# Performance work log

Measured on AMD Instinct MI355X. Metric: run time of the kernel, lower is better.

## Reference

```python
import jax, jax.numpy as jnp
import numpy as np

# Dia-style ANE decoder dims
B, D, S = 2, 2048, 128          # batch, n_embd, query seqlen
A, T = 1536, 512                # audio_length (self KV cache), text_length (cross KV)
HQ, HKV, HD = 16, 4, 128        # gqa query heads, kv heads, gqa head dim
HC, HDC = 16, 128               # cross-attn heads / head dim (encoder n_head/head_dim)
FF, L = 8192, 2                 # mlp hidden, n_layers
NEG = -3e4                      # large-negative additive mask (stands in for -inf)
EPS = 1e-5


def _rmsnorm(x, w):
    # x: (B, D, S); ANERMSNorm normalizes over channel dim (dim=1)
    inv = jax.lax.rsqrt(jnp.mean(x * x, axis=1, keepdims=True) + EPS)
    return x * inv * w[None, :, None]


def _rope(x, sin, cos):
    # x: (B, H, hd, S); sin/cos: (B, 1, hd//2, S) -- split-half rotary
    h = x.shape[2] // 2
    x1, x2 = x[:, :, :h], x[:, :, h:]
    return jnp.concatenate([x1 * cos - x2 * sin, x2 * cos + x1 * sin], axis=2)


def setup_inputs() -> dict:
    key = jax.random.key(0)
    ks = jax.random.split(key, 16)
    w0 = 256  # KV cache write position
    x = jax.random.normal(ks[0], (B, D, 1, S), jnp.float32)
    positions = (w0 + jnp.arange(S, dtype=jnp.int32))[None, :].repeat(B, axis=0)
    kv_write_index = jnp.array([w0], dtype=jnp.int32)
    # additive causal mask over cache positions: allow cache_pos <= w0 + q_pos
    allowed = jnp.arange(A)[None, :] <= (w0 + jnp.arange(S))[:, None]  # (S, A)
    self_attn_mask = jnp.where(allowed, 0.0, NEG).astype(jnp.float32)[None, None].repeat(B, axis=0)
    encoder_lengths = jnp.full((B, 1), 384, dtype=jnp.int32)
    sc = 0.02
    return {
        'x': x, 'positions': positions, 'kv_write_index': kv_write_index,
        'self_attn_mask': self_attn_mask, 'encoder_lengths': encoder_lengths,
        'q_w': jax.random.normal(ks[1], (L, D, HQ * HD)) * sc,
        'k_w': jax.random.normal(ks[2], (L, D, HKV * HD)) * sc,
        'v_w': jax.random.normal(ks[3], (L, D, HKV * HD)) * sc,
        'o_w': jax.random.normal(ks[4], (L, HQ * HD, D)) * sc,
        'cq_w': jax.random.normal(ks[5], (L, D, HC * HDC)) * sc,
        'co_w': jax.random.normal(ks[6], (L, HC * HDC, D)) * sc,
        'sa_norm_w': jnp.ones((L, D)), 'ca_norm_w': jnp.ones((L, D)),
        'mlp_norm_w': jnp.ones((L, D)), 'final_norm_w': jnp.ones((D,)),
        'wg_w': jax.random.normal(ks[7], (L, D, FF)) * sc,
        'wu_w': jax.random.normal(ks[8], (L, D, FF)) * sc,
        'wd_w': jax.random.normal(ks[9], (L, FF, D)) * sc,
        'k_cache': jax.random.normal(ks[10], (L * B, HKV, A, HD)) * 0.1,
        'v_cache': jax.random.normal(ks[11], (L * B, HKV, HD, A)) * 0.1,
        'ck_cache': jax.random.normal(ks[12], (L * B, HC, T, HDC)) * 0.1,
        'cv_cache': jax.random.normal(ks[13], (L * B, HC, HDC, T)) * 0.1,
    }


def _forward(x4, positions, kv_write_index, self_attn_mask, encoder_lengths,
             q_w, k_w, v_w, o_w, cq_w, co_w, sa_norm_w, ca_norm_w, mlp_norm_w,
             final_norm_w, wg_w, wu_w, wd_w, k_cache, v_cache, ck_cache, cv_cache):
    x = x4[:, :, 0, :]  # (B, D, S) channels-first ANE layout
    w = kv_write_index[0]
    # rotary tables from positions
    inv_freq = 1.0 / (10000.0 ** (jnp.arange(0, HD, 2, dtype=jnp.float32) / HD))
    ang = positions.astype(jnp.float32)[:, None, :] * inv_freq[None, :, None]  # (B, HD/2, S)
    sin, cos = jnp.sin(ang)[:, None], jnp.cos(ang)[:, None]  # (B,1,HD/2,S)
    sa_mask = jnp.swapaxes(self_attn_mask, -1, -2)  # (B,1,A,S), additive
    # cross-attn key padding mask from encoder lengths (non-causal)
    k_valid = jnp.arange(T)[None, :] < encoder_lengths[:, 0:1]  # (B, T)
    ca_mask = jnp.where(k_valid, 0.0, NEG).astype(x.dtype)[:, None, :, None]  # (B,1,T,1)
    scale = 1.0 / np.sqrt(HD).astype(np.float32)
    cscale = 1.0 / np.sqrt(HDC).astype(np.float32)
    G = HQ // HKV
    for l in range(L):
        # ---- self attention with RoPE + KV-cache write ----
        h = _rmsnorm(x, sa_norm_w[l])
        q = jnp.einsum('bds,de->bes', h, q_w[l]).reshape(B, HQ, HD, S)
        k = jnp.einsum('bds,de->bes', h, k_w[l]).reshape(B, HKV, HD, S)
        v = jnp.einsum('bds,de->bes', h, v_w[l]).reshape(B, HKV, HD, S)
        q = _rope(q, sin, cos)
        k = jnp.swapaxes(_rope(k, sin, cos), -1, -2)  # (B,HKV,S,HD)
        k_cache = jax.lax.dynamic_update_slice(k_cache, k, (l * B, 0, w, 0))
        v_cache = jax.lax.dynamic_update_slice(v_cache, v, (l * B, 0, 0, w))
        key = k_cache[l * B:(l + 1) * B]   # (B,HKV,A,HD)
        val = v_cache[l * B:(l + 1) * B]   # (B,HKV,HD,A)
        qg = q.reshape(B, HKV, G, HD, S)
        scores = jnp.einsum('bkad,bkgds->bkgas', key, qg) * scale
        probs = jax.nn.softmax(scores + sa_mask[:, :, None], axis=3)
        attn = jnp.einsum('bkda,bkgas->bkgds', val, probs).reshape(B, HQ * HD, S)
        x = x + jnp.einsum('bes,ed->bds', attn, o_w[l])
        # ---- cross attention (precomputed encoder KV cache, RoPE on q) ----
        h = _rmsnorm(x, ca_norm_w[l])
        q = jnp.einsum('bds,de->bes', h, cq_w[l]).reshape(B, HC, HDC, S)
        q = _rope(q, sin, cos)
        ckey = ck_cache[l * B:(l + 1) * B]  # (B,HC,T,HDC)
        cval = cv_cache[l * B:(l + 1) * B]  # (B,HC,HDC,T)
        cscores = jnp.einsum('bhtd,bhds->bhts', ckey, q) * cscale
        cprobs = jax.nn.softmax(cscores + ca_mask, axis=2)
        cattn = jnp.einsum('bhdt,bhts->bhds', cval, cprobs).reshape(B, HC * HDC, S)
        x = x + jnp.einsum('bes,ed->bds', cattn, co_w[l])
        # ---- SwiGLU MLP ----
        h = _rmsnorm(x, mlp_norm_w[l])
        gate = jnp.einsum('bds,df->bfs', h, wg_w[l])
        up = jnp.einsum('bds,df->bfs', h, wu_w[l])
        x = x + jnp.einsum('bfs,fd->bds', jax.nn.silu(gate) * up, wd_w[l])
    x = _rmsnorm(x, final_norm_w)
    return x[:, :, None, :]


def reference(x, positions, kv_write_index, self_attn_mask, encoder_lengths,
              q_w, k_w, v_w, o_w, cq_w, co_w, sa_norm_w, ca_norm_w, mlp_norm_w,
              final_norm_w, wg_w, wu_w, wd_w, k_cache, v_cache, ck_cache, cv_cache):
    return _forward(x, positions, kv_write_index, self_attn_mask, encoder_lengths,
                    q_w, k_w, v_w, o_w, cq_w, co_w, sa_norm_w, ca_norm_w, mlp_norm_w,
                    final_norm_w, wg_w, wu_w, wd_w, k_cache, v_cache, ck_cache, cv_cache)
```

## Files before the change

kernel.cpp:

```cpp
#include <hip/hip_runtime.h>
#include <math.h>
#include <stdint.h>

namespace {

constexpr int B_ = 2, D_ = 2048, S_ = 128, A_ = 1536, T_ = 512;
constexpr int HQ_ = 16, HKV_ = 4, HD_ = 128, FF_ = 8192, L_ = 2;
constexpr float NEG_ = -30000.0f, EPS_ = 1e-5f;
constexpr int TOK_ = B_ * S_;

typedef __attribute__((ext_vector_type(4))) float f32x4;
typedef __attribute__((ext_vector_type(8))) short s16x8;

__device__ __forceinline__ uint32_t bf16pair(float x) {
  uint32_t xi = __float_as_uint(x);
  uint32_t hi = (xi + 0x7FFFu + ((xi >> 16) & 1u)) >> 16;
  float hf = __uint_as_float(hi << 16);
  float r = x - hf;
  uint32_t ri = __float_as_uint(r);
  uint32_t lo = (ri + 0x7FFFu + ((ri >> 16) & 1u)) >> 16;
  return (hi & 0xFFFFu) | (lo << 16);
}

__device__ __forceinline__ void unpack8(uint4 q0, uint4 q1, s16x8& hi, s16x8& lo) {
  union U { uint32_t w[4]; s16x8 v; };
  U h, l;
  uint32_t u[8] = {q0.x, q0.y, q0.z, q0.w, q1.x, q1.y, q1.z, q1.w};
#pragma unroll
  for (int r = 0; r < 4; r++) {
    h.w[r] = __builtin_amdgcn_perm(u[2 * r + 1], u[2 * r], 0x05040100u);
    l.w[r] = __builtin_amdgcn_perm(u[2 * r + 1], u[2 * r], 0x07060302u);
  }
  hi = h.v;
  lo = l.v;
}

__global__ __launch_bounds__(256) void rms_sumsq(const float* __restrict__ x,
                                                 float* __restrict__ rsum) {
  int b = blockIdx.y, c = blockIdx.x;
  int tid = threadIdx.x;
  int s = tid & 127, dd = tid >> 7;
  const float* xp = x + ((size_t)b * D_ + c * 128) * S_ + s;
  float acc = 0.f;
  for (int d = dd; d < 128; d += 2) {
    float v = xp[(size_t)d * S_];
    acc += v * v;
  }
  __shared__ float lds[256];
  lds[tid] = acc;
  __syncthreads();
  if (dd == 0) atomicAdd(&rsum[b * S_ + s], lds[s] + lds[128 + s]);
}

__global__ __launch_bounds__(256) void rms_apply(const float* __restrict__ x,
                                                 const float* __restrict__ rsum,
                                                 const float* __restrict__ w,
                                                 float* __restrict__ out) {
  int i = blockIdx.x * 256 + threadIdx.x;
  int s = i & (S_ - 1);
  int d = (i / S_) & (D_ - 1);
  int b = i / (D_ * S_);
  float inv = rsqrtf(rsum[b * S_ + s] * (1.0f / D_) + EPS_);
  out[i] = x[i] * inv * w[d];
}

__global__ __launch_bounds__(256) void pack_h(const float* __restrict__ H,
                                              uint32_t* __restrict__ Ht, int K) {
  int b = blockIdx.y;
  int k0 = blockIdx.x * 64;
  __shared__ uint32_t t[128][65];
  int tid = threadIdx.x;
  int s = tid & 127, kk = tid >> 7;
  const float* Hp = H + ((size_t)b * K + k0) * S_ + s;
  for (int k = kk; k < 64; k += 2) t[s][k] = bf16pair(Hp[(size_t)k * S_]);
  __syncthreads();
  int k2 = tid & 63, s2 = tid >> 6;
  uint32_t* Op = Ht + (size_t)(b * S_) * K + k0 + k2;
  for (int ss = s2; ss < 128; ss += 4) Op[(size_t)ss * K] = t[ss][k2];
}

__global__ __launch_bounds__(256, 2) void gemm_mfma(
    const float* __restrict__ W, const uint32_t* __restrict__ Ht,
    float* __restrict__ Out, int M, int K, int KC, int accum) {
  __shared__ uint32_t As[128 * 32];
  __shared__ uint32_t Bs[128 * 32];
  int m0 = blockIdx.x * 128;
  int b = blockIdx.y;
  int k0 = blockIdx.z * KC;
  int tid = threadIdx.x;
  int lane = tid & 63, wave = tid >> 6;
  int wm = (wave >> 1) * 64, wn = (wave & 1) * 64;
  int lr = lane & 15, lg = lane >> 4;
  int a_k4 = (tid >> 5) * 4;
  int a_m4 = (tid & 31) * 4;
  int ag = a_k4 >> 2;
  int b_g = tid & 3;
  int b_s = tid >> 2;
  const uint32_t* HtB = Ht + (size_t)(b * S_) * K;

  f32x4 acc[4][4];
  f32x4 zero = {0.f, 0.f, 0.f, 0.f};
#pragma unroll
  for (int i = 0; i < 4; i++)
#pragma unroll
    for (int j = 0; j < 4; j++) acc[i][j] = zero;

  for (int kk = k0; kk < k0 + KC; kk += 32) {
    const float* Wp = W + (size_t)(kk + a_k4) * M + (m0 + a_m4);
    float4 w0 = *(const float4*)(Wp);
    float4 w1 = *(const float4*)(Wp + (size_t)M);
    float4 w2 = *(const float4*)(Wp + 2 * (size_t)M);
    float4 w3 = *(const float4*)(Wp + 3 * (size_t)M);
    {
      uint4 u;
      int m = a_m4;
      u.x = bf16pair(w0.x); u.y = bf16pair(w1.x); u.z = bf16pair(w2.x); u.w = bf16pair(w3.x);
      *(uint4*)&As[m * 32 + ((ag ^ (m & 7)) << 2)] = u;
      m = a_m4 + 1;
      u.x = bf16pair(w0.y); u.y = bf16pair(w1.y); u.z = bf16pair(w2.y); u.w = bf16pair(w3.y);
      *(uint4*)&As[m * 32 + ((ag ^ (m & 7)) << 2)] = u;
      m = a_m4 + 2;
      u.x = bf16pair(w0.z); u.y = bf16pair(w1.z); u.z = bf16pair(w2.z); u.w = bf16pair(w3.z);
      *(uint4*)&As[m * 32 + ((ag ^ (m & 7)) << 2)] = u;
      m = a_m4 + 3;
      u.x = bf16pair(w0.w); u.y = bf16pair(w1.w); u.z = bf16pair(w2.w); u.w = bf16pair(w3.w);
      *(uint4*)&As[m * 32 + ((ag ^ (m & 7)) << 2)] = u;
    }
#pragma unroll
    for (int c = 0; c < 2; c++)
#pragma unroll
      for (int d = 0; d < 2; d++) {
        int s = b_s + c * 64;
        int g = b_g + d * 4;
        uint4 v = *(const uint4*)&HtB[(size_t)s * K + kk + g * 4];
        *(uint4*)&Bs[s * 32 + ((g ^ (s & 7)) << 2)] = v;
      }
    __syncthreads();
    s16x8 ah[4], al[4], bhf[4], blf[4];
#pragma unroll
    for (int mi = 0; mi < 4; mi++) {
      int row = wm + mi * 16 + lr;
      const uint32_t* p = &As[row * 32];
      uint4 q0 = *(const uint4*)&p[(((lg << 1) ^ (row & 7)) << 2)];
      uint4 q1 = *(const uint4*)&p[((((lg << 1) | 1) ^ (row & 7)) << 2)];
      unpack8(q0, q1, ah[mi], al[mi]);
    }
#pragma unroll
    for (int ni = 0; ni < 4; ni++) {
      int row = wn + ni * 16 + lr;
      const uint32_t* p = &Bs[row * 32];
      uint4 q0 = *(const uint4*)&p[(((lg << 1) ^ (row & 7)) << 2)];
      uint4 q1 = *(const uint4*)&p[((((lg << 1) | 1) ^ (row & 7)) << 2)];
      unpack8(q0, q1, bhf[ni], blf[ni]);
    }
#pragma unroll
    for (int mi = 0; mi < 4; mi++)
#pragma unroll
      for (int ni = 0; ni < 4; ni++)
        acc[mi][ni] = __builtin_amdgcn_mfma_f32_16x16x32_bf16(ah[mi], bhf[ni],
                                                              acc[mi][ni], 0, 0, 0);
#pragma unroll
    for (int mi = 0; mi < 4; mi++)
#pragma unroll
      for (int ni = 0; ni < 4; ni++)
        acc[mi][ni] = __builtin_amdgcn_mfma_f32_16x16x32_bf16(ah[mi], blf[ni],
                                                              acc[mi][ni], 0, 0, 0);
#pragma unroll
    for (int mi = 0; mi < 4; mi++)
#pragma unroll
      for (int ni = 0; ni < 4; ni++)
        acc[mi][ni] = __builtin_amdgcn_mfma_f32_16x16x32_bf16(al[mi], bhf[ni],
                                                              acc[mi][ni], 0, 0, 0);
    __syncthreads();
  }
  if (gridDim.z == 1) {
#pragma unroll
    for (int mi = 0; mi < 4; mi++)
#pragma unroll
      for (int ni = 0; ni < 4; ni++) {
        int m = m0 + wm + mi * 16 + lg * 4;
        int sI = wn + ni * 16 + lr;
        size_t base = ((size_t)b * M + m) * S_ + sI;
#pragma unroll
        for (int r = 0; r < 4; r++) {
          float v = acc[mi][ni][r];
          if (accum) v += Out[base + (size_t)r * S_];
          Out[base + (size_t)r * S_] = v;
        }
      }
  } else {
#pragma unroll
    for (int mi = 0; mi < 4; mi++)
#pragma unroll
      for (int ni = 0; ni < 4; ni++) {
        int m = m0 + wm + mi * 16 + lg * 4;
        int sI = wn + ni * 16 + lr;
        size_t base = ((size_t)b * M + m) * S_ + sI;
#pragma unroll
        for (int r = 0; r < 4; r++)
          atomicAdd(&Out[base + (size_t)r * S_], acc[mi][ni][r]);
      }
  }
}

__global__ __launch_bounds__(256, 2) void attn_scores_mfma(
    const float* __restrict__ key, const uint32_t* __restrict__ Qt,
    float* __restrict__ P, const float* __restrict__ maskArr,
    const int* __restrict__ encLen, const int* __restrict__ wptr, float scale,
    int gshift, int AN, int mode) {
  int bh = blockIdx.y;
  int b = bh >> 4, h = bh & 15;
  int kvh = h >> gshift, nkv = 16 >> gshift;
  int Aeff = (mode == 0) ? (wptr[0] + S_) : T_;
  int a0 = blockIdx.x * 128;
  if (a0 >= Aeff) return;
  __shared__ uint32_t As[128 * 32];
  __shared__ uint32_t Bs[128 * 32];
  const float* kbase =
      key + (size_t)(b * nkv + kvh) * AN * HD_ + (size_t)a0 * HD_;
  const uint32_t* qbase = Qt + (size_t)(b * S_) * D_ + h * HD_;
  int tid = threadIdx.x, lane = tid & 63, wave = tid >> 6;
  int wm = (wave >> 1) * 64, wn = (wave & 1) * 64;
  int lr = lane & 15, lg = lane >> 4;
  int g_ = tid & 3, r_ = tid >> 2;

  f32x4 acc[4][4];
  f32x4 zero = {0.f, 0.f, 0.f, 0.f};
#pragma unroll
  for (int i = 0; i < 4; i++)
#pragma unroll
    for (int j = 0; j < 4; j++) acc[i][j] = zero;

  for (int hc = 0; hc < HD_; hc += 32) {
#pragma unroll
    for (int c = 0; c < 2; c++)
#pragma unroll
      for (int d = 0; d < 2; d++) {
        int row = r_ + c * 64, g = g_ + d * 4;
        float4 v = *(const float4*)&kbase[(size_t)row * HD_ + hc + g * 4];
        uint4 u;
        u.x = bf16pair(v.x); u.y = bf16pair(v.y);
        u.z = bf16pair(v.z); u.w = bf16pair(v.w);
        *(uint4*)&As[row * 32 + ((g ^ (row & 7)) << 2)] = u;
        uint4 q = *(const uint4*)&qbase[(size_t)row * D_ + hc + g * 4];
        *(uint4*)&Bs[row * 32 + ((g ^ (row & 7)) << 2)] = q;
      }
    __syncthreads();
    s16x8 ah[4], al[4], bhf[4], blf[4];
#pragma unroll
    for (int mi = 0; mi < 4; mi++) {
      int row = wm + mi * 16 + lr;
      const uint32_t* p = &As[row * 32];
      uint4 q0 = *(const uint4*)&p[(((lg << 1) ^ (row & 7)) << 2)];
      uint4 q1 = *(const uint4*)&p[((((lg << 1) | 1) ^ (row & 7)) << 2)];
      unpack8(q0, q1, ah[mi], al[mi]);
    }
#pragma unroll
    for (int ni = 0; ni < 4; ni++) {
      int row = wn + ni * 16 + lr;
      const uint32_t* p = &Bs[row * 32];
      uint4 q0 = *(const uint4*)&p[(((lg << 1) ^ (row & 7)) << 2)];
      uint4 q1 = *(const uint4*)&p[((((lg << 1) | 1) ^ (row & 7)) << 2)];
      unpack8(q0, q1, bhf[ni], blf[ni]);
    }
#pragma unroll
    for (int mi = 0; mi < 4; mi++)
#pragma unroll
      for (int ni = 0; ni < 4; ni++)
        acc[mi][ni] = __builtin_amdgcn_mfma_f32_16x16x32_bf16(ah[mi], bhf[ni],
                                                              acc[mi][ni], 0, 0, 0);
#pragma unroll
    for (int mi = 0; mi < 4; mi++)
#pragma unroll
      for (int ni = 0; ni < 4; ni++)
        acc[mi][ni] = __builtin_amdgcn_mfma_f32_16x16x32_bf16(ah[mi], blf[ni],
                                                              acc[mi][ni], 0, 0, 0);
#pragma unroll
    for (int mi = 0; mi < 4; mi++)
#pragma unroll
      for (int ni = 0; ni < 4; ni++)
        acc[mi][ni] = __builtin_amdgcn_mfma_f32_16x16x32_bf16(al[mi], bhf[ni],
                                                              acc[mi][ni], 0, 0, 0);
    __syncthreads();
  }
  int eLen = (mode == 0) ? 0 : encLen[b];
#pragma unroll
  for (int mi = 0; mi < 4; mi++)
#pragma unroll
    for (int ni = 0; ni < 4; ni++) {
      int ab = a0 + wm + mi * 16 + lg * 4;
      int s = wn + ni * 16 + lr;
      float* Pp = P + ((size_t)bh * S_ + s) * T_;
      const float* Mp = maskArr + ((size_t)b * S_ + s) * A_;
#pragma unroll
      for (int r = 0; r < 4; r++) {
        int a = ab + r;
        if (a < Aeff) {
          float mval = (mode == 0) ? Mp[a] : ((a < eLen) ? 0.f : NEG_);
          Pp[a] = acc[mi][ni][r] * scale + mval;
        }
      }
    }
}

__global__ __launch_bounds__(256, 2) void attn_pv_mfma(
    const float* __restrict__ val, const float* __restrict__ P,
    float* __restrict__ out, const int* __restrict__ wptr, int gshift, int AN,
    int mode) {
  int bh = blockIdx.x;
  int b = bh >> 4, h = bh & 15;
  int kvh = h >> gshift, nkv = 16 >> gshift;
  int Aeff = (mode == 0) ? (wptr[0] + S_) : T_;
  int nk = (Aeff + 31) >> 5;
  __shared__ uint32_t As[128 * 32];
  __shared__ uint32_t Bs[128 * 32];
  const float* vbase = val + (size_t)(b * nkv + kvh) * HD_ * AN;
  const float* Pb = P + (size_t)bh * S_ * T_;
  int tid = threadIdx.x, lane = tid & 63, wave = tid >> 6;
  int wm = (wave >> 1) * 64, wn = (wave & 1) * 64;
  int lr = lane & 15, lg = lane >> 4;
  int g_ = tid & 3, r_ = tid >> 2;

  f32x4 acc[4][4];
  f32x4 zero = {0.f, 0.f, 0.f, 0.f};
#pragma unroll
  for (int i = 0; i < 4; i++)
#pragma unroll
    for (int j = 0; j < 4; j++) acc[i][j] = zero;

  for (int kkt = 0; kkt < nk; kkt++) {
    int a0c = kkt * 32;
#pragma unroll
    for (int c = 0; c < 2; c++)
#pragma unroll
      for (int d = 0; d < 2; d++) {
        int row = r_ + c * 64, g = g_ + d * 4;
        int a = a0c + g * 4;
        float4 v = *(const float4*)&vbase[(size_t)row * AN + a];
        uint4 u;
        u.x = bf16pair(v.x); u.y = bf16pair(v.y);
        u.z = bf16pair(v.z); u.w = bf16pair(v.w);
        *(uint4*)&As[row * 32 + ((g ^ (row & 7)) << 2)] = u;
        float4 p4 = *(const float4*)&Pb[(size_t)row * T_ + a];
        uint4 up;
        up.x = (a + 0 < Aeff) ? bf16pair(p4.x) : 0u;
        up.y = (a + 1 < Aeff) ? bf16pair(p4.y) : 0u;
        up.z = (a + 2 < Aeff) ? bf16pair(p4.z) : 0u;
        up.w = (a + 3 < Aeff) ? bf16pair(p4.w) : 0u;
        *(uint4*)&Bs[row * 32 + ((g ^ (row & 7)) << 2)] = up;
      }
    __syncthreads();
    s16x8 ah[4], al[4], bhf[4], blf[4];
#pragma unroll
    for (int mi = 0; mi < 4; mi++) {
      int row = wm + mi * 16 + lr;
      const uint32_t* p = &As[row * 32];
      uint4 q0 = *(const uint4*)&p[(((lg << 1) ^ (row & 7)) << 2)];
      uint4 q1 = *(const uint4*)&p[((((lg << 1) | 1) ^ (row & 7)) << 2)];
      unpack8(q0, q1, ah[mi], al[mi]);
    }
#pragma unroll
    for (int ni = 0; ni < 4; ni++) {
      int row = wn + ni * 16 + lr;
      const uint32_t* p = &Bs[row * 32];
      uint4 q0 = *(const uint4*)&p[(((lg << 1) ^ (row & 7)) << 2)];
      uint4 q1 = *(const uint4*)&p[((((lg << 1) | 1) ^ (row & 7)) << 2)];
      unpack8(q0, q1, bhf[ni], blf[ni]);
    }
#pragma unroll
    for (int mi = 0; mi < 4; mi++)
#pragma unroll
      for (int ni = 0; ni < 4; ni++)
        acc[mi][ni] = __builtin_amdgcn_mfma_f32_16x16x32_bf16(ah[mi], bhf[ni],
                                                              acc[mi][ni], 0, 0, 0);
#pragma unroll
    for (int mi = 0; mi < 4; mi++)
#pragma unroll
      for (int ni = 0; ni < 4; ni++)
        acc[mi][ni] = __builtin_amdgcn_mfma_f32_16x16x32_bf16(ah[mi], blf[ni],
                                                              acc[mi][ni], 0, 0, 0);
#pragma unroll
    for (int mi = 0; mi < 4; mi++)
#pragma unroll
      for (int ni = 0; ni < 4; ni++)
        acc[mi][ni] = __builtin_amdgcn_mfma_f32_16x16x32_bf16(al[mi], bhf[ni],
                                                              acc[mi][ni], 0, 0, 0);
    __syncthreads();
  }
#pragma unroll
  for (int mi = 0; mi < 4; mi++)
#pragma unroll
    for (int ni = 0; ni < 4; ni++) {
      int hd = wm + mi * 16 + lg * 4;
      int s = wn + ni * 16 + lr;
      size_t base = ((size_t)bh * HD_ + hd) * S_ + s;
#pragma unroll
      for (int r = 0; r < 4; r++) out[base + (size_t)r * S_] = acc[mi][ni][r];
    }
}

__device__ __forceinline__ void rope_angles(int pos, int i, float& sn, float& cs) {
  float inv_freq = powf(10000.0f, -(float)i * (1.0f / 64.0f));
  float ang = (float)pos * inv_freq;
  sn = sinf(ang);
  cs = cosf(ang);
}

__global__ __launch_bounds__(256) void rope_q(float* __restrict__ q,
                                              const int* __restrict__ positions) {
  int idx = blockIdx.x * 256 + threadIdx.x;
  int s = idx & 127;
  int i = (idx >> 7) & 63;
  int b = idx >> 17;
  float sn, cs;
  rope_angles(positions[b * S_ + s], i, sn, cs);
  size_t o1 = (size_t)(idx >> 13) * (128 * S_) + (size_t)i * S_ + s;
  float x1 = q[o1], x2 = q[o1 + 64 * S_];
  q[o1] = x1 * cs - x2 * sn;
  q[o1 + 64 * S_] = x2 * cs + x1 * sn;
}

__global__ __launch_bounds__(256) void rope_k_store(const float* __restrict__ kbuf,
                                                    const int* __restrict__ positions,
                                                    const int* __restrict__ wptr,
                                                    float* __restrict__ k_cache, int l) {
  int idx = blockIdx.x * 256 + threadIdx.x;
  int i = idx & 63;
  int s = (idx >> 6) & 127;
  int kv = (idx >> 13) & 3;
  int b = idx >> 15;
  int w = wptr[0];
  float sn, cs;
  rope_angles(positions[b * S_ + s], i, sn, cs);
  size_t i1 = ((size_t)(b * HKV_ + kv) * HD_ + i) * S_ + s;
  float x1 = kbuf[i1], x2 = kbuf[i1 + 64 * S_];
  size_t o = ((size_t)((l * B_ + b) * HKV_ + kv) * A_ + (w + s)) * HD_ + i;
  k_cache[o] = x1 * cs - x2 * sn;
  k_cache[o + 64] = x2 * cs + x1 * sn;
}

__global__ __launch_bounds__(256) void store_v(const float* __restrict__ vbuf,
                                               const int* __restrict__ wptr,
                                               float* __restrict__ v_cache, int l) {
  int idx = blockIdx.x * 256 + threadIdx.x;
  int s = idx & 127;
  int hd = (idx >> 7) & 127;
  int kv = (idx >> 14) & 3;
  int b = idx >> 16;
  int w = wptr[0];
  v_cache[((size_t)((l * B_ + b) * HKV_ + kv) * HD_ + hd) * A_ + w + s] = vbuf[idx];
}

__global__ __launch_bounds__(128) void softmax_rows(float* __restrict__ P,
                                                    const int* __restrict__ wptr,
                                                    int mode) {
  int row = blockIdx.x;
  int Aeff = (mode == 0) ? (wptr[0] + S_) : T_;
  float* p = P + (size_t)row * T_;
  int tid = threadIdx.x;
  float v[4];
  int cnt = 0;
  float m = -1e30f;
  for (int a = tid; a < Aeff; a += 128) {
    float t = p[a];
    v[cnt++] = t;
    m = fmaxf(m, t);
  }
  __shared__ float r0[2], r1[2];
  for (int off = 32; off > 0; off >>= 1) m = fmaxf(m, __shfl_down(m, off));
  if ((tid & 63) == 0) r0[tid >> 6] = m;
  __syncthreads();
  m = fmaxf(r0[0], r0[1]);
  float sum = 0.f;
  for (int i = 0; i < cnt; i++) {
    v[i] = expf(v[i] - m);
    sum += v[i];
  }
  for (int off = 32; off > 0; off >>= 1) sum += __shfl_down(sum, off);
  if ((tid & 63) == 0) r1[tid >> 6] = sum;
  __syncthreads();
  float inv = 1.f / (r1[0] + r1[1]);
  cnt = 0;
  for (int a = tid; a < Aeff; a += 128) p[a] = v[cnt++] * inv;
}

__global__ __launch_bounds__(256) void silu_mul(float* __restrict__ gate,
                                                const float* __restrict__ up) {
  int i = blockIdx.x * 256 + threadIdx.x;
  float g = gate[i];
  gate[i] = g / (1.f + expf(-g)) * up[i];
}

}

extern "C" void kernel_launch(void* const* d_in, const int* in_sizes, int n_in,
                              void* d_out, int out_size, void* d_ws, size_t ws_size,
                              hipStream_t stream) {
  const float* x_in = (const float*)d_in[0];
  const int* positions = (const int*)d_in[1];
  const int* wptr = (const int*)d_in[2];
  const float* maskArr = (const float*)d_in[3];
  const int* encLen = (const int*)d_in[4];
  const float* q_w = (const float*)d_in[5];
  const float* k_w = (const float*)d_in[6];
  const float* v_w = (const float*)d_in[7];
  const float* o_w = (const float*)d_in[8];
  const float* cq_w = (const float*)d_in[9];
  const float* co_w = (const float*)d_in[10];
  const float* sa_norm = (const float*)d_in[11];
  const float* ca_norm = (const float*)d_in[12];
  const float* mlp_norm = (const float*)d_in[13];
  const float* fin_norm = (const float*)d_in[14];
  const float* wg_w = (const float*)d_in[15];
  const float* wu_w = (const float*)d_in[16];
  const float* wd_w = (const float*)d_in[17];
  float* k_cache = (float*)d_in[18];
  float* v_cache = (float*)d_in[19];
  const float* ck_cache = (const float*)d_in[20];
  const float* cv_cache = (const float*)d_in[21];
  float* out = (float*)d_out;

  float* ws = (float*)d_ws;
  const size_t BDS = (size_t)B_ * D_ * S_;
  float* X = ws;
  float* Hb = X + BDS;
  float* Q = Hb + BDS;
  float* Attn = Q + BDS;
  float* Kb = Attn + BDS;
  float* Vb = Kb + (size_t)B_ * 512 * S_;
  float* Pbuf = Vb + (size_t)B_ * 512 * S_;
  float* Up = Pbuf + (size_t)B_ * 16 * S_ * T_;
  float* Rsum = Up + (size_t)B_ * FF_ * S_;
  uint32_t* Ht = (uint32_t*)(Rsum + B_ * S_);

  const float scale = 0.08838834764831845f;

  hipMemcpyAsync(X, x_in, BDS * sizeof(float), hipMemcpyDeviceToDevice, stream);

  auto rms = [&](const float* src, const float* w, float* dst) {
    hipMemsetAsync(Rsum, 0, B_ * S_ * sizeof(float), stream);
    rms_sumsq<<<dim3(16, B_), 256, 0, stream>>>(src, Rsum);
    rms_apply<<<dim3(B_ * D_ * S_ / 256), 256, 0, stream>>>(src, Rsum, w, dst);
  };
  auto pack = [&](const float* src, int K) {
    pack_h<<<dim3(K / 64, B_), 256, 0, stream>>>(src, Ht, K);
  };
  auto mgemm = [&](const float* Wm, float* Outm, int M, int K, int SK, int accum,
                   int zero) {
    if (zero)
      hipMemsetAsync(Outm, 0, (size_t)B_ * M * S_ * sizeof(float), stream);
    gemm_mfma<<<dim3(M / 128, B_, SK), 256, 0, stream>>>(Wm, Ht, Outm, M, K, K / SK,
                                                         accum);
  };

  for (int l = 0; l < L_; l++) {
    rms(X, sa_norm + (size_t)l * D_, Hb);
    pack(Hb, D_);
    mgemm(q_w + (size_t)l * D_ * 2048, Q, 2048, D_, 4, 0, 1);
    mgemm(k_w + (size_t)l * D_ * 512, Kb, 512, D_, 8, 0, 1);
    mgemm(v_w + (size_t)l * D_ * 512, Vb, 512, D_, 8, 0, 1);
    rope_q<<<dim3(B_ * 16 * 64 * S_ / 256), 256, 0, stream>>>(Q, positions);
    rope_k_store<<<dim3(B_ * 4 * S_ * 64 / 256), 256, 0, stream>>>(Kb, positions, wptr,
                                                                   k_cache, l);
    store_v<<<dim3(B_ * 4 * 128 * S_ / 256), 256, 0, stream>>>(Vb, wptr, v_cache, l);
    pack(Q, D_);
    attn_scores_mfma<<<dim3(4, B_ * 16), 256, 0, stream>>>(
        k_cache + (size_t)l * B_ * HKV_ * A_ * HD_, Ht, Pbuf, maskArr, encLen, wptr,
        scale, 2, A_, 0);
    softmax_rows<<<dim3(B_ * 16 * S_), 128, 0, stream>>>(Pbuf, wptr, 0);
    attn_pv_mfma<<<dim3(B_ * 16), 256, 0, stream>>>(
        v_cache + (size_t)l * B_ * HKV_ * HD_ * A_, Pbuf, Attn, wptr, 2, A_, 0);
    pack(Attn, D_);
    mgemm(o_w + (size_t)l * 2048 * D_, X, D_, 2048, 4, 1, 0);
    rms(X, ca_norm + (size_t)l * D_, Hb);
    pack(Hb, D_);
    mgemm(cq_w + (size_t)l * D_ * 2048, Q, 2048, D_, 4, 0, 1);
    rope_q<<<dim3(B_ * 16 * 64 * S_ / 256), 256, 0, stream>>>(Q, positions);
    pack(Q, D_);
    attn_scores_mfma<<<dim3(4, B_ * 16), 256, 0, stream>>>(
        ck_cache + (size_t)l * B_ * 16 * T_ * HD_, Ht, Pbuf, maskArr, encLen, wptr,
        scale, 0, T_, 1);
    softmax_rows<<<dim3(B_ * 16 * S_), 128, 0, stream>>>(Pbuf, wptr, 1);
    attn_pv_mfma<<<dim3(B_ * 16), 256, 0, stream>>>(
        cv_cache + (size_t)l * B_ * 16 * HD_ * T_, Pbuf, Attn, wptr, 0, T_, 1);
    pack(Attn, D_);
    mgemm(co_w + (size_t)l * 2048 * D_, X, D_, 2048, 4, 1, 0);
    rms(X, mlp_norm + (size_t)l * D_, Hb);
    pack(Hb, D_);
    mgemm(wg_w + (size_t)l * D_ * FF_, Pbuf, FF_, D_, 2, 0, 1);
    mgemm(wu_w + (size_t)l * D_ * FF_, Up, FF_, D_, 2, 0, 1);
    silu_mul<<<dim3(B_ * FF_ * S_ / 256), 256, 0, stream>>>(Pbuf, Up);
    pack(Pbuf, FF_);
    mgemm(wd_w + (size_t)l * FF_ * D_, X, D_, FF_, 8, 1, 0);
  }
  rms(X, fin_norm, out);
}
```

Measured before the change: 1.819 ms.

## Fuse QKV and gate/up GEMMs and fold rmsnorm, rope, silu into packing

The GEMM kernel now selects among up to three weight matrices by tile index, so Q/K/V run as one launch and gate/up as another, writing into concatenated output buffers. RMSNorm application, query RoPE and SiLU-multiply are folded into the bf16 transpose-pack kernels, which removes the standalone elementwise passes and their float round trips through memory. Split-K factors change as well: QKV and the output projections use 8 splits and the cross-query projection now uses 8. More atomics from the extra split-K add contention, and the pack kernels now recompute sin/cos per element.

```diff
diff --git a/kernel.cpp b/kernel.cpp
--- a/kernel.cpp
+++ b/kernel.cpp
@@ -7,7 +7,6 @@
 constexpr int B_ = 2, D_ = 2048, S_ = 128, A_ = 1536, T_ = 512;
 constexpr int HQ_ = 16, HKV_ = 4, HD_ = 128, FF_ = 8192, L_ = 2;
 constexpr float NEG_ = -30000.0f, EPS_ = 1e-5f;
-constexpr int TOK_ = B_ * S_;
 
 typedef __attribute__((ext_vector_type(4))) float f32x4;
 typedef __attribute__((ext_vector_type(8))) short s16x8;
@@ -33,6 +32,13 @@
   }
   hi = h.v;
   lo = l.v;
+}
+
+__device__ __forceinline__ void rope_angles(int pos, int i, float& sn, float& cs) {
+  float inv_freq = powf(10000.0f, -(float)i * (1.0f / 64.0f));
+  float ang = (float)pos * inv_freq;
+  sn = sinf(ang);
+  cs = cosf(ang);
 }
 
 __global__ __launch_bounds__(256) void rms_sumsq(const float* __restrict__ x,
@@ -79,12 +85,84 @@
   for (int ss = s2; ss < 128; ss += 4) Op[(size_t)ss * K] = t[ss][k2];
 }
 
+__global__ __launch_bounds__(256) void pack_rms(const float* __restrict__ H,
+                                                const float* __restrict__ rsum,
+                                                const float* __restrict__ w,
+                                                uint32_t* __restrict__ Ht) {
+  int b = blockIdx.y;
+  int k0 = blockIdx.x * 64;
+  __shared__ uint32_t t[128][65];
+  int tid = threadIdx.x;
+  int s = tid & 127, kk = tid >> 7;
+  const float* Hp = H + ((size_t)b * D_ + k0) * S_ + s;
+  float inv = rsqrtf(rsum[b * S_ + s] * (1.0f / D_) + EPS_);
+  for (int k = kk; k < 64; k += 2)
+    t[s][k] = bf16pair(Hp[(size_t)k * S_] * inv * w[k0 + k]);
+  __syncthreads();
+  int k2 = tid & 63, s2 = tid >> 6;
+  uint32_t* Op = Ht + (size_t)(b * S_) * D_ + k0 + k2;
+  for (int ss = s2; ss < 128; ss += 4) Op[(size_t)ss * D_] = t[ss][k2];
+}
+
+__global__ __launch_bounds__(256) void pack_rope(const float* __restrict__ QKV,
+                                                 const int* __restrict__ positions,
+                                                 uint32_t* __restrict__ Ht) {
+  int b = blockIdx.y, c = blockIdx.x;
+  int h = c >> 1, half = c & 1, k0 = c * 64;
+  __shared__ uint32_t t[128][65];
+  int tid = threadIdx.x;
+  int s = tid & 127, kk = tid >> 7;
+  const float* Qp = QKV + ((size_t)b * 3072 + h * 128) * S_ + s;
+  int pos = positions[b * S_ + s];
+  for (int i = kk; i < 64; i += 2) {
+    float sn, cs;
+    rope_angles(pos, i, sn, cs);
+    float x1 = Qp[(size_t)i * S_], x2 = Qp[(size_t)(i + 64) * S_];
+    t[s][i] = bf16pair(half == 0 ? x1 * cs - x2 * sn : x2 * cs + x1 * sn);
+  }
+  __syncthreads();
+  int k2 = tid & 63, s2 = tid >> 6;
+  uint32_t* Op = Ht + (size_t)(b * S_) * D_ + k0 + k2;
+  for (int ss = s2; ss < 128; ss += 4) Op[(size_t)ss * D_] = t[ss][k2];
+}
+
+__global__ __launch_bounds__(256) void pack_silu(const float* __restrict__ GU,
+                                                 uint32_t* __restrict__ Ht) {
+  int b = blockIdx.y;
+  int k0 = blockIdx.x * 64;
+  __shared__ uint32_t t[128][65];
+  int tid = threadIdx.x;
+  int s = tid & 127, kk = tid >> 7;
+  const float* Gp = GU + ((size_t)b * 16384 + k0) * S_ + s;
+  const float* Up2 = Gp + (size_t)8192 * S_;
+  for (int k = kk; k < 64; k += 2) {
+    float g = Gp[(size_t)k * S_], u = Up2[(size_t)k * S_];
+    t[s][k] = bf16pair(g / (1.f + expf(-g)) * u);
+  }
+  __syncthreads();
+  int k2 = tid & 63, s2 = tid >> 6;
+  uint32_t* Op = Ht + (size_t)(b * S_) * FF_ + k0 + k2;
+  for (int ss = s2; ss < 128; ss += 4) Op[(size_t)ss * FF_] = t[ss][k2];
+}
+
 __global__ __launch_bounds__(256, 2) void gemm_mfma(
-    const float* __restrict__ W, const uint32_t* __restrict__ Ht,
-    float* __restrict__ Out, int M, int K, int KC, int accum) {
+    const float* __restrict__ W0, const float* __restrict__ W1,
+    const float* __restrict__ W2, int tb1, int tb2, int Mw0, int Mw1, int Mw2,
+    const uint32_t* __restrict__ Ht, float* __restrict__ Out, int MS, int K,
+    int KC, int accum) {
   __shared__ uint32_t As[128 * 32];
   __shared__ uint32_t Bs[128 * 32];
-  int m0 = blockIdx.x * 128;
+  int mt = blockIdx.x;
+  int m0 = mt * 128;
+  const float* W;
+  int Mw, mW;
+  if (mt < tb1) {
+    W = W0; Mw = Mw0; mW = m0;
+  } else if (mt < tb2) {
+    W = W1; Mw = Mw1; mW = m0 - tb1 * 128;
+  } else {
+    W = W2; Mw = Mw2; mW = m0 - tb2 * 128;
+  }
   int b = blockIdx.y;
   int k0 = blockIdx.z * KC;
   int tid = threadIdx.x;
@@ -106,11 +184,11 @@
     for (int j = 0; j < 4; j++) acc[i][j] = zero;
 
   for (int kk = k0; kk < k0 + KC; kk += 32) {
-    const float* Wp = W + (size_t)(kk + a_k4) * M + (m0 + a_m4);
+    const float* Wp = W + (size_t)(kk + a_k4) * Mw + (mW + a_m4);
     float4 w0 = *(const float4*)(Wp);
-    float4 w1 = *(const float4*)(Wp + (size_t)M);
-    float4 w2 = *(const float4*)(Wp + 2 * (size_t)M);
-    float4 w3 = *(const float4*)(Wp + 3 * (size_t)M);
+    float4 w1 = *(const float4*)(Wp + (size_t)Mw);
+    float4 w2 = *(const float4*)(Wp + 2 * (size_t)Mw);
+    float4 w3 = *(const float4*)(Wp + 3 * (size_t)Mw);
     {
       uint4 u;
       int m = a_m4;
@@ -180,7 +258,7 @@
       for (int ni = 0; ni < 4; ni++) {
         int m = m0 + wm + mi * 16 + lg * 4;
         int sI = wn + ni * 16 + lr;
-        size_t base = ((size_t)b * M + m) * S_ + sI;
+        size_t base = ((size_t)b * MS + m) * S_ + sI;
 #pragma unroll
         for (int r = 0; r < 4; r++) {
           float v = acc[mi][ni][r];
@@ -195,7 +273,7 @@
       for (int ni = 0; ni < 4; ni++) {
         int m = m0 + wm + mi * 16 + lg * 4;
         int sI = wn + ni * 16 + lr;
-        size_t base = ((size_t)b * M + m) * S_ + sI;
+        size_t base = ((size_t)b * MS + m) * S_ + sI;
 #pragma unroll
         for (int r = 0; r < 4; r++)
           atomicAdd(&Out[base + (size_t)r * S_], acc[mi][ni][r]);
@@ -399,28 +477,7 @@
     }
 }
 
-__device__ __forceinline__ void rope_angles(int pos, int i, float& sn, float& cs) {
-  float inv_freq = powf(10000.0f, -(float)i * (1.0f / 64.0f));
-  float ang = (float)pos * inv_freq;
-  sn = sinf(ang);
-  cs = cosf(ang);
-}
-
-__global__ __launch_bounds__(256) void rope_q(float* __restrict__ q,
-                                              const int* __restrict__ positions) {
-  int idx = blockIdx.x * 256 + threadIdx.x;
-  int s = idx & 127;
-  int i = (idx >> 7) & 63;
-  int b = idx >> 17;
-  float sn, cs;
-  rope_angles(positions[b * S_ + s], i, sn, cs);
-  size_t o1 = (size_t)(idx >> 13) * (128 * S_) + (size_t)i * S_ + s;
-  float x1 = q[o1], x2 = q[o1 + 64 * S_];
-  q[o1] = x1 * cs - x2 * sn;
-  q[o1 + 64 * S_] = x2 * cs + x1 * sn;
-}
-
-__global__ __launch_bounds__(256) void rope_k_store(const float* __restrict__ kbuf,
+__global__ __launch_bounds__(256) void rope_k_store(const float* __restrict__ QKV,
                                                     const int* __restrict__ positions,
                                                     const int* __restrict__ wptr,
                                                     float* __restrict__ k_cache, int l) {
@@ -432,14 +489,14 @@
   int w = wptr[0];
   float sn, cs;
   rope_angles(positions[b * S_ + s], i, sn, cs);
-  size_t i1 = ((size_t)(b * HKV_ + kv) * HD_ + i) * S_ + s;
-  float x1 = kbuf[i1], x2 = kbuf[i1 + 64 * S_];
+  size_t i1 = ((size_t)b * 3072 + 2048 + kv * 128 + i) * S_ + s;
+  float x1 = QKV[i1], x2 = QKV[i1 + (size_t)64 * S_];
   size_t o = ((size_t)((l * B_ + b) * HKV_ + kv) * A_ + (w + s)) * HD_ + i;
   k_cache[o] = x1 * cs - x2 * sn;
   k_cache[o + 64] = x2 * cs + x1 * sn;
 }
 
-__global__ __launch_bounds__(256) void store_v(const float* __restrict__ vbuf,
+__global__ __launch_bounds__(256) void store_v(const float* __restrict__ QKV,
                                                const int* __restrict__ wptr,
                                                float* __restrict__ v_cache, int l) {
   int idx = blockIdx.x * 256 + threadIdx.x;
@@ -448,7 +505,8 @@
   int kv = (idx >> 14) & 3;
   int b = idx >> 16;
   int w = wptr[0];
-  v_cache[((size_t)((l * B_ + b) * HKV_ + kv) * HD_ + hd) * A_ + w + s] = vbuf[idx];
+  float v = QKV[((size_t)b * 3072 + 2560 + kv * 128 + hd) * S_ + s];
+  v_cache[((size_t)((l * B_ + b) * HKV_ + kv) * HD_ + hd) * A_ + w + s] = v;
 }
 
 __global__ __launch_bounds__(128) void softmax_rows(float* __restrict__ P,
@@ -482,13 +540,6 @@
   float inv = 1.f / (r1[0] + r1[1]);
   cnt = 0;
   for (int a = tid; a < Aeff; a += 128) p[a] = v[cnt++] * inv;
-}
-
-__global__ __launch_bounds__(256) void silu_mul(float* __restrict__ gate,
-                                                const float* __restrict__ up) {
-  int i = blockIdx.x * 256 + threadIdx.x;
-  float g = gate[i];
-  gate[i] = g / (1.f + expf(-g)) * up[i];
 }
 
 }
@@ -523,75 +574,73 @@
   float* ws = (float*)d_ws;
   const size_t BDS = (size_t)B_ * D_ * S_;
   float* X = ws;
-  float* Hb = X + BDS;
-  float* Q = Hb + BDS;
-  float* Attn = Q + BDS;
-  float* Kb = Attn + BDS;
-  float* Vb = Kb + (size_t)B_ * 512 * S_;
-  float* Pbuf = Vb + (size_t)B_ * 512 * S_;
-  float* Up = Pbuf + (size_t)B_ * 16 * S_ * T_;
-  float* Rsum = Up + (size_t)B_ * FF_ * S_;
-  uint32_t* Ht = (uint32_t*)(Rsum + B_ * S_);
+  float* QKV = X + BDS;
+  float* Attn = QKV + (size_t)B_ * 3072 * S_;
+  float* GU = Attn + BDS;
+  float* Pbuf = GU;
+  float* Rsum = GU + (size_t)B_ * 16384 * S_;
+  uint32_t* Ht = (uint32_t*)(Rsum + 1024);
 
   const float scale = 0.08838834764831845f;
+  const int BIG = 1 << 30;
 
   hipMemcpyAsync(X, x_in, BDS * sizeof(float), hipMemcpyDeviceToDevice, stream);
 
-  auto rms = [&](const float* src, const float* w, float* dst) {
+  auto norm_pack = [&](const float* src, const float* w) {
     hipMemsetAsync(Rsum, 0, B_ * S_ * sizeof(float), stream);
     rms_sumsq<<<dim3(16, B_), 256, 0, stream>>>(src, Rsum);
-    rms_apply<<<dim3(B_ * D_ * S_ / 256), 256, 0, stream>>>(src, Rsum, w, dst);
+    pack_rms<<<dim3(32, B_), 256, 0, stream>>>(src, Rsum, w, Ht);
   };
-  auto pack = [&](const float* src, int K) {
-    pack_h<<<dim3(K / 64, B_), 256, 0, stream>>>(src, Ht, K);
-  };
-  auto mgemm = [&](const float* Wm, float* Outm, int M, int K, int SK, int accum,
-                   int zero) {
-    if (zero)
-      hipMemsetAsync(Outm, 0, (size_t)B_ * M * S_ * sizeof(float), stream);
-    gemm_mfma<<<dim3(M / 128, B_, SK), 256, 0, stream>>>(Wm, Ht, Outm, M, K, K / SK,
-                                                         accum);
-  };
 
   for (int l = 0; l < L_; l++) {
-    rms(X, sa_norm + (size_t)l * D_, Hb);
-    pack(Hb, D_);
-    mgemm(q_w + (size_t)l * D_ * 2048, Q, 2048, D_, 4, 0, 1);
-    mgemm(k_w + (size_t)l * D_ * 512, Kb, 512, D_, 8, 0, 1);
-    mgemm(v_w + (size_t)l * D_ * 512, Vb, 512, D_, 8, 0, 1);
-    rope_q<<<dim3(B_ * 16 * 64 * S_ / 256), 256, 0, stream>>>(Q, positions);
-    rope_k_store<<<dim3(B_ * 4 * S_ * 64 / 256), 256, 0, stream>>>(Kb, positions, wptr,
-                                                                   k_cache, l);
-    store_v<<<dim3(B_ * 4 * 128 * S_ / 256), 256, 0, stream>>>(Vb, wptr, v_cache, l);
-    pack(Q, D_);
+    norm_pack(X, sa_norm + (size_t)l * D_);
+    hipMemsetAsync(QKV, 0, (size_t)B_ * 3072 * S_ * sizeof(float), stream);
+    gemm_mfma<<<dim3(24, B_, 8), 256, 0, stream>>>(
+        q_w + (size_t)l * D_ * 2048, k_w + (size_t)l * D_ * 512,
+        v_w + (size_t)l * D_ * 512, 16, 20, 2048, 512, 512, Ht, QKV, 3072, D_,
+        D_ / 8, 0);
+    rope_k_store<<<dim3(B_ * 4 * 128 * 64 / 256), 256, 0, stream>>>(
+        QKV, positions, wptr, k_cache, l);
+    store_v<<<dim3(B_ * 4 * 128 * 128 / 256), 256, 0, stream>>>(QKV, wptr, v_cache,
+                                                                l);
+    pack_rope<<<dim3(32, B_), 256, 0, stream>>>(QKV, positions, Ht);
     attn_scores_mfma<<<dim3(4, B_ * 16), 256, 0, stream>>>(
         k_cache + (size_t)l * B_ * HKV_ * A_ * HD_, Ht, Pbuf, maskArr, encLen, wptr,
         scale, 2, A_, 0);
     softmax_rows<<<dim3(B_ * 16 * S_), 128, 0, stream>>>(Pbuf, wptr, 0);
     attn_pv_mfma<<<dim3(B_ * 16), 256, 0, stream>>>(
         v_cache + (size_t)l * B_ * HKV_ * HD_ * A_, Pbuf, Attn, wptr, 2, A_, 0);
-    pack(Attn, D_);
-    mgemm(o_w + (size_t)l * 2048 * D_, X, D_, 2048, 4, 1, 0);
-    rms(X, ca_norm + (size_t)l * D_, Hb);
-    pack(Hb, D_);
-    mgemm(cq_w + (size_t)l * D_ * 2048, Q, 2048, D_, 4, 0, 1);
-    rope_q<<<dim3(B_ * 16 * 64 * S_ / 256), 256, 0, stream>>>(Q, positions);
-    pack(Q, D_);
+    pack_h<<<dim3(32, B_), 256, 0, stream>>>(Attn, Ht, D_);
+    gemm_mfma<<<dim3(16, B_, 8), 256, 0, stream>>>(
+        o_w + (size_t)l * 2048 * D_, nullptr, nullptr, BIG, BIG, 2048, 0, 0, Ht, X,
+        2048, 2048, 2048 / 8, 1);
+    norm_pack(X, ca_norm + (size_t)l * D_);
+    hipMemsetAsync(QKV, 0, (size_t)B_ * 3072 * S_ * sizeof(float), stream);
+    gemm_mfma<<<dim3(16, B_, 8), 256, 0, stream>>>(
+        cq_w + (size_t)l * D_ * 2048, nullptr, nullptr, BIG, BIG, 2048, 0, 0, Ht,
+        QKV, 3072, D_, D_ / 8, 0);
+    pack_rope<<<dim3(32, B_), 256, 0, stream>>>(QKV, positions, Ht);
     attn_scores_mfma<<<dim3(4, B_ * 16), 256, 0, stream>>>(
         ck_cache + (size_t)l * B_ * 16 * T_ * HD_, Ht, Pbuf, maskArr, encLen, wptr,
         scale, 0, T_, 1);
     softmax_rows<<<dim3(B_ * 16 * S_), 128, 0, stream>>>(Pbuf, wptr, 1);
     attn_pv_mfma<<<dim3(B_ * 16), 256, 0, stream>>>(
         cv_cache + (size_t)l * B_ * 16 * HD_ * T_, Pbuf, Attn, wptr, 0, T_, 1);
-    pack(Attn, D_);
-    mgemm(co_w + (size_t)l * 2048 * D_, X, D_, 2048, 4, 1, 0);
-    rms(X, mlp_norm + (size_t)l * D_, Hb);
-    pack(Hb, D_);
-    mgemm(wg_w + (size_t)l * D_ * FF_, Pbuf, FF_, D_, 2, 0, 1);
-    mgemm(wu_w + (size_t)l * D_ * FF_, Up, FF_, D_, 2, 0, 1);
-    silu_mul<<<dim3(B_ * FF_ * S_ / 256), 256, 0, stream>>>(Pbuf, Up);
-    pack(Pbuf, FF_);
-    mgemm(wd_w + (size_t)l * FF_ * D_, X, D_, FF_, 8, 1, 0);
-  }
-  rms(X, fin_norm, out);
-}
+    pack_h<<<dim3(32, B_), 256, 0, stream>>>(Attn, Ht, D_);
+    gemm_mfma<<<dim3(16, B_, 8), 256, 0, stream>>>(
+        co_w + (size_t)l * 2048 * D_, nullptr, nullptr, BIG, BIG, 2048, 0, 0, Ht, X,
+        2048, 2048, 2048 / 8, 1);
+    norm_pack(X, mlp_norm + (size_t)l * D_);
+    hipMemsetAsync(GU, 0, (size_t)B_ * 16384 * S_ * sizeof(float), stream);
+    gemm_mfma<<<dim3(128, B_, 2), 256, 0, stream>>>(
+        wg_w + (size_t)l * D_ * FF_, wu_w + (size_t)l * D_ * FF_, nullptr, 64, BIG,
+        8192, 8192, 0, Ht, GU, 16384, D_, D_ / 2, 0);
+    pack_silu<<<dim3(128, B_), 256, 0, stream>>>(GU, Ht);
+    gemm_mfma<<<dim3(16, B_, 8), 256, 0, stream>>>(
+        wd_w + (size_t)l * FF_ * D_, nullptr, nullptr, BIG, BIG, 2048, 0, 0, Ht, X,
+        2048, FF_, FF_ / 8, 1);
+  }
+  hipMemsetAsync(Rsum, 0, B_ * S_ * sizeof(float), stream);
+  rms_sumsq<<<dim3(16, B_), 256, 0, stream>>>(X, Rsum);
+  rms_apply<<<dim3(B_ * D_ * S_ / 256), 256, 0, stream>>>(X, Rsum, fin_norm, out);
+}
```

Result: faster. 1.630 ms (-10.4%).
